# Optimization experiments

Hardware: AMD Instinct MI355X
Metric: run time of the kernel (lower is better)

Reference implementation:

```python
import jax, jax.numpy as jnp
import numpy as np

B, S, H, D_MODEL, D_HEAD = 2, 2048, 12, 768, 64
INIT_RANGE = 0.02
IGNORE = -100000.0


def setup_inputs() -> dict:
    key = jax.random.key(0)
    ks = jax.random.split(key, 11)
    return {
        "normalized_resid_pre_q": jax.random.normal(ks[0], (B, S, H, D_MODEL), jnp.float32),
        "normalized_resid_pre_k": jax.random.normal(ks[1], (B, S, H, D_MODEL), jnp.float32),
        "normalized_resid_pre_v": jax.random.normal(ks[2], (B, S, H, D_MODEL), jnp.float32),
        "W_Q": jax.random.normal(ks[3], (H, D_MODEL, D_HEAD), jnp.float32) * INIT_RANGE,
        "b_Q": jnp.zeros((H, D_HEAD), jnp.float32),
        "W_K": jax.random.normal(ks[4], (H, D_MODEL, D_HEAD), jnp.float32) * INIT_RANGE,
        "b_K": jnp.zeros((H, D_HEAD), jnp.float32),
        "W_V": jax.random.normal(ks[5], (H, D_MODEL, D_HEAD), jnp.float32) * INIT_RANGE,
        "b_V": jnp.zeros((H, D_HEAD), jnp.float32),
        "W_O": jax.random.normal(ks[6], (H, D_HEAD, D_MODEL), jnp.float32) * INIT_RANGE,
        "b_O": jnp.zeros((D_MODEL,), jnp.float32),
    }


def reference(normalized_resid_pre_q, normalized_resid_pre_k, normalized_resid_pre_v,
              W_Q, b_Q, W_K, b_K, W_V, b_V, W_O, b_O):
    n_heads = W_Q.shape[0]
    d_head = W_Q.shape[-1]
    # per-head projections: input already carries a head axis
    q = jnp.einsum("bqhm,hmd->bqhd", normalized_resid_pre_q, W_Q) + b_Q
    k = jnp.einsum("bkhm,hmd->bkhd", normalized_resid_pre_k, W_K) + b_K
    v = jnp.einsum("bkhm,hmd->bkhd", normalized_resid_pre_v, W_V) + b_V
    scores = jnp.einsum("bqhd,bkhd->bhqk", q, k) / jnp.sqrt(jnp.float32(d_head))
    S_q, S_k = scores.shape[-2], scores.shape[-1]
    causal = jnp.triu(jnp.ones((S_q, S_k), bool), k=1)
    scores = jnp.where(causal, jnp.float32(IGNORE), scores)
    pattern = jax.nn.softmax(scores, axis=-1)
    z = jnp.einsum("bhqk,bkhd->bqhd", pattern, v)
    # output keeps the per-head axis; bias split evenly across heads
    attn_out = jnp.einsum("bqhd,hdm->bqhm", z, W_O) + b_O / n_heads
    return attn_out
```

## Files before the change

kernel.cpp:

```cpp
#include <hip/hip_runtime.h>
#include <hip/hip_bf16.h>
#include <stdint.h>

#define H 12
#define S 2048
#define BATCH 2
#define DM 768
#define DH 64

typedef __attribute__((ext_vector_type(4))) float f32x4;
typedef __attribute__((ext_vector_type(8))) short s16x8;

static __device__ __forceinline__ short f2bf(float f) {
  uint32_t u = __builtin_bit_cast(uint32_t, f);
  uint32_t r = (u + 0x7FFFu + ((u >> 16) & 1u)) >> 16;
  return (short)r;
}

static __device__ __forceinline__ s16x8 cvt8(f32x4 a, f32x4 b) {
  s16x8 r;
  r[0] = f2bf(a[0]); r[1] = f2bf(a[1]); r[2] = f2bf(a[2]); r[3] = f2bf(a[3]);
  r[4] = f2bf(b[0]); r[5] = f2bf(b[1]); r[6] = f2bf(b[2]); r[7] = f2bf(b[3]);
  return r;
}

static __device__ __forceinline__ f32x4 zero4() {
  f32x4 v; v[0] = 0.f; v[1] = 0.f; v[2] = 0.f; v[3] = 0.f; return v;
}

static __device__ __forceinline__ int xcd_swz(int lin, int n) {
  int q = n >> 3;
  return (lin & 7) * q + (lin >> 3);
}

#define GLD_LDS16(g, l)                                                              \
  __builtin_amdgcn_global_load_lds((__attribute__((address_space(1))) const void*)(g), \
                                   (__attribute__((address_space(3))) void*)(l), 16, 0, 0)

#define WAITV(N) asm volatile("s_waitcnt vmcnt(" #N ")" ::: "memory")
#define WAITL0() asm volatile("s_waitcnt lgkmcnt(0)" ::: "memory")
#define BAR() __builtin_amdgcn_s_barrier()
#define FENCE() asm volatile("" ::: "memory")

__global__ __launch_bounds__(256) void k_prep(const float* __restrict__ wq,
                                              const float* __restrict__ wk,
                                              const float* __restrict__ wv,
                                              const float* __restrict__ wo,
                                              short* __restrict__ wt,
                                              short* __restrict__ wot) {
  int tid = blockIdx.x * 256 + threadIdx.x;
  int nthr = gridDim.x * 256;
  const int NQKV = 3 * H * DM * DH;
  for (int i = tid; i < NQKV; i += nthr) {
    int n = i & 63;
    int k = (i >> 6) % DM;
    int rest = (i >> 6) / DM;
    int h = rest % H;
    int t = rest / H;
    const float* src = (t == 0 ? wq : t == 1 ? wk : wv);
    float v = src[((size_t)h * DM + k) * DH + n];
    wt[(((size_t)t * H + h) * DH + n) * DM + k] = f2bf(v);
  }
  const int NO = H * DH * DM;
  for (int i = tid; i < NO; i += nthr) {
    int m = i % DM;
    int d = (i / DM) % DH;
    int h = i / (DM * DH);
    wot[((size_t)h * DM + m) * DH + d] = f2bf(wo[((size_t)h * DH + d) * DM + m]);
  }
}

__global__ __launch_bounds__(256) void k_proj(
    const float* __restrict__ xq, const float* __restrict__ xk, const float* __restrict__ xv,
    const float* __restrict__ bq, const float* __restrict__ bk, const float* __restrict__ bv,
    const short* __restrict__ wt,
    short* __restrict__ q_ws, short* __restrict__ k_ws, short* __restrict__ vt_ws) {
  int lin = blockIdx.x + 64 * (blockIdx.y + 12 * blockIdx.z);
  lin = xcd_swz(lin, 64 * 12 * 3);
  const int t = lin / (64 * 12);
  const int h = (lin >> 6) % 12;
  const int b = (lin & 63) >> 5;
  const int q0 = (lin & 31) * 64;

  const float* x = (t == 0 ? xq : t == 1 ? xk : xv);
  const float* xbase = x + ((size_t)(b * S + q0) * H + h) * DM;
  const short* wbase = wt + ((size_t)t * H + h) * (size_t)DH * DM;

  __shared__ float A_sm[2][64 * 64];
  __shared__ short W_sm[2][64 * 64];

  const int tid = threadIdx.x;
  const int w = tid >> 6;
  const int l = tid & 63;
  const int g = l >> 4;
  const int m16 = l & 15;
  const int wswz = ((l & 7) ^ (l >> 3)) * 8;

  const int arow_st = (l >> 4);
  const int apb = (l & 15) * 16;

  f32x4 acc[4];
#pragma unroll
  for (int nt = 0; nt < 4; ++nt) acc[nt] = zero4();

#define PROJ_STAGE(sel, kc)                                                          \
  do {                                                                               \
    _Pragma("unroll") for (int i = 0; i < 4; ++i) {                                  \
      int row = (w * 4 + i) * 4 + arow_st;                                           \
      int colf = (apb ^ ((row & 7) << 4)) >> 2;                                      \
      GLD_LDS16(xbase + (size_t)row * (H * DM) + (kc) * 64 + colf,                   \
                (char*)A_sm + (sel) * 16384 + (w * 4 + i) * 1024);                   \
    }                                                                                \
    _Pragma("unroll") for (int i = 0; i < 2; ++i) {                                  \
      int ch = w * 2 + i;                                                            \
      int n = ch * 8 + (l >> 3);                                                     \
      GLD_LDS16(wbase + (size_t)n * DM + (kc) * 64 + wswz,                           \
                (char*)W_sm + (sel) * 8192 + ch * 1024);                             \
    }                                                                                \
  } while (0)

#define PROJ_COMPUTE(sel)                                                            \
  do {                                                                               \
    const char* Ab = (const char*)A_sm + (sel) * 16384;                              \
    const char* Wb = (const char*)W_sm + (sel) * 8192;                               \
    int arow = 16 * w + m16;                                                         \
    int asw = (arow & 7) << 4;                                                       \
    _Pragma("unroll") for (int c = 0; c < 2; ++c) {                                  \
      f32x4 a0 = *(const f32x4*)(Ab + arow * 256 + ((32 * g + 128 * c) ^ asw));      \
      f32x4 a1 = *(const f32x4*)(Ab + arow * 256 + ((32 * g + 128 * c + 16) ^ asw)); \
      s16x8 afr = cvt8(a0, a1);                                                      \
      int krow = 8 * g + 32 * c;                                                     \
      _Pragma("unroll") for (int nt = 0; nt < 4; ++nt) {                             \
        int n = m16 + 16 * nt;                                                       \
        s16x8 bfr = *(const s16x8*)(Wb + ((n * 128 + krow * 2) ^ ((n & 7) << 4)));   \
        acc[nt] = __builtin_amdgcn_mfma_f32_16x16x32_bf16(afr, bfr, acc[nt], 0, 0, 0); \
      }                                                                              \
    }                                                                                \
  } while (0)

  PROJ_STAGE(0, 0);
#pragma unroll
  for (int kc = 0; kc < 12; ++kc) {
    const int cur = kc & 1;
    if (kc < 11) {
      PROJ_STAGE(cur ^ 1, kc + 1);
      WAITV(6);
    } else {
      WAITV(0);
    }
    BAR(); FENCE();
    PROJ_COMPUTE(cur);
    WAITL0(); BAR(); FENCE();
  }

  const float* bias = (t == 0 ? bq : t == 1 ? bk : bv) + h * DH;
  if (t < 2) {
    short* dst = (t == 0 ? q_ws : k_ws) + (size_t)(b * H + h) * S * DH;
#pragma unroll
    for (int nt = 0; nt < 4; ++nt) {
      int n = 16 * nt + m16;
      float bb = bias[n];
#pragma unroll
      for (int r = 0; r < 4; ++r) {
        int q = q0 + 16 * w + 4 * g + r;
        dst[(size_t)q * DH + n] = f2bf(acc[nt][r] + bb);
      }
    }
  } else {
    short* dst = vt_ws + (size_t)(b * H + h) * DH * S;
#pragma unroll
    for (int nt = 0; nt < 4; ++nt) {
      int n = 16 * nt + m16;
      float bb = bias[n];
#pragma unroll
      for (int r = 0; r < 4; ++r) {
        int q = q0 + 16 * w + 4 * g + r;
        dst[(size_t)n * S + q] = f2bf(acc[nt][r] + bb);
      }
    }
  }
}

__global__ __launch_bounds__(256) void k_attn(const short* __restrict__ q_ws,
                                              const short* __restrict__ k_ws,
                                              const short* __restrict__ vt_ws,
                                              short* __restrict__ z_ws) {
  int lin = blockIdx.x + 32 * (blockIdx.y + 12 * blockIdx.z);
  lin = xcd_swz(lin, 32 * 12 * 2);
  const int q0 = (lin & 31) * 64;
  const int h = (lin >> 5) % 12;
  const int b = lin / (32 * 12);

  const size_t sl = (size_t)(b * H + h) * S * DH;
  const short* qs = q_ws + sl;
  const short* ks = k_ws + sl;
  const short* vs = vt_ws + sl;
  short* zs = z_ws + sl;

  __shared__ short K_sm[2][64 * 64];
  __shared__ short V_sm[2][64 * 64];
  __shared__ short P_sm[4][16 * 72];

  const int tid = threadIdx.x;
  const int w = tid >> 6;
  const int l = tid & 63;
  const int g = l >> 4;
  const int m16 = l & 15;
  const int swz_src = ((l & 7) ^ (l >> 3)) * 8;

#define ATTN_STAGE(sel, kv0)                                                         \
  do {                                                                               \
    _Pragma("unroll") for (int i = 0; i < 2; ++i) {                                  \
      int ch = w * 2 + i;                                                            \
      int row = ch * 8 + (l >> 3);                                                   \
      GLD_LDS16(ks + (size_t)((kv0) + row) * DH + swz_src,                           \
                (char*)K_sm + (sel) * 8192 + ch * 1024);                             \
      GLD_LDS16(vs + (size_t)row * S + (kv0) + swz_src,                              \
                (char*)V_sm + (sel) * 8192 + ch * 1024);                             \
    }                                                                                \
  } while (0)

  s16x8 qf[2];
  {
    int q = q0 + 16 * w + m16;
    qf[0] = *(const s16x8*)(qs + (size_t)q * DH + 8 * g);
    qf[1] = *(const s16x8*)(qs + (size_t)q * DH + 8 * g + 32);
  }

  f32x4 o_acc[4];
  float m_run[4], l_run[4], alpha[4];
#pragma unroll
  for (int nt = 0; nt < 4; ++nt) o_acc[nt] = zero4();
#pragma unroll
  for (int r = 0; r < 4; ++r) { m_run[r] = -3.0e38f; l_run[r] = 0.f; }

  const int ktiles = (q0 >> 6) + 1;
  ATTN_STAGE(0, 0);
  for (int kt = 0; kt < ktiles; ++kt) {
    const int kv0 = kt * 64;
    const int cur = kt & 1;
    if (kt + 1 < ktiles) {
      ATTN_STAGE(cur ^ 1, kv0 + 64);
      WAITV(4);
    } else {
      WAITV(0);
    }
    BAR(); FENCE();

    f32x4 sacc[4];
#pragma unroll
    for (int nt = 0; nt < 4; ++nt) sacc[nt] = zero4();
#pragma unroll
    for (int c = 0; c < 2; ++c) {
      int kr2 = (8 * g + 32 * c) * 2;
#pragma unroll
      for (int nt = 0; nt < 4; ++nt) {
        int row = m16 + 16 * nt;
        s16x8 kf = *(const s16x8*)((const char*)K_sm + cur * 8192 +
                                   ((row * 128 + kr2) ^ ((row & 7) << 4)));
        sacc[nt] = __builtin_amdgcn_mfma_f32_16x16x32_bf16(qf[c], kf, sacc[nt], 0, 0, 0);
      }
    }
    float sv[4][4];
#pragma unroll
    for (int nt = 0; nt < 4; ++nt) {
      int kv = kv0 + 16 * nt + m16;
#pragma unroll
      for (int r = 0; r < 4; ++r) {
        int q = q0 + 16 * w + 4 * g + r;
        float s = sacc[nt][r] * 0.125f;
        sv[nt][r] = (kv > q) ? -1.0e30f : s;
      }
    }
#pragma unroll
    for (int r = 0; r < 4; ++r) {
      float tm = fmaxf(fmaxf(sv[0][r], sv[1][r]), fmaxf(sv[2][r], sv[3][r]));
      tm = fmaxf(tm, __shfl_xor(tm, 1));
      tm = fmaxf(tm, __shfl_xor(tm, 2));
      tm = fmaxf(tm, __shfl_xor(tm, 4));
      tm = fmaxf(tm, __shfl_xor(tm, 8));
      float mn = fmaxf(m_run[r], tm);
      alpha[r] = __expf(m_run[r] - mn);
      m_run[r] = mn;
      float rs = 0.f;
#pragma unroll
      for (int nt = 0; nt < 4; ++nt) {
        float p = __expf(sv[nt][r] - mn);
        sv[nt][r] = p;
        rs += p;
      }
      rs += __shfl_xor(rs, 1);
      rs += __shfl_xor(rs, 2);
      rs += __shfl_xor(rs, 4);
      rs += __shfl_xor(rs, 8);
      l_run[r] = l_run[r] * alpha[r] + rs;
    }
#pragma unroll
    for (int nt = 0; nt < 4; ++nt)
#pragma unroll
      for (int r = 0; r < 4; ++r)
        P_sm[w][(4 * g + r) * 72 + 16 * nt + m16] = f2bf(sv[nt][r]);
#pragma unroll
    for (int nt = 0; nt < 4; ++nt)
#pragma unroll
      for (int r = 0; r < 4; ++r) o_acc[nt][r] *= alpha[r];
#pragma unroll
    for (int c = 0; c < 2; ++c) {
      s16x8 pf = *(const s16x8*)(&P_sm[w][m16 * 72 + 8 * g + 32 * c]);
      int kv2 = (8 * g + 32 * c) * 2;
#pragma unroll
      for (int nt = 0; nt < 4; ++nt) {
        int d = m16 + 16 * nt;
        s16x8 vf = *(const s16x8*)((const char*)V_sm + cur * 8192 +
                                   ((d * 128 + kv2) ^ ((d & 7) << 4)));
        o_acc[nt] = __builtin_amdgcn_mfma_f32_16x16x32_bf16(pf, vf, o_acc[nt], 0, 0, 0);
      }
    }
    WAITL0(); BAR(); FENCE();
  }
#pragma unroll
  for (int nt = 0; nt < 4; ++nt) {
    int d = 16 * nt + m16;
#pragma unroll
    for (int r = 0; r < 4; ++r) {
      int q = q0 + 16 * w + 4 * g + r;
      zs[(size_t)q * DH + d] = f2bf(o_acc[nt][r] / l_run[r]);
    }
  }
}

__global__ __launch_bounds__(256) void k_oproj(const short* __restrict__ z_ws,
                                               const short* __restrict__ wot,
                                               const float* __restrict__ bo,
                                               float* __restrict__ out) {
  int lin = blockIdx.x + 32 * (blockIdx.y + 12 * blockIdx.z);
  lin = xcd_swz(lin, 32 * 12 * 2);
  const int q0 = (lin & 31) * 64;
  const int h = (lin >> 5) % 12;
  const int b = lin / (32 * 12);

  const short* zs = z_ws + (size_t)(b * H + h) * S * DH;
  const short* wos = wot + (size_t)h * DM * DH;

  __shared__ short Z_sm[64 * 64];
  __shared__ short W_sm[2][128 * 64];

  const int tid = threadIdx.x;
  const int w = tid >> 6;
  const int l = tid & 63;
  const int g = l >> 4;
  const int m16 = l & 15;
  const int swz_src = ((l & 7) ^ (l >> 3)) * 8;

#define OPROJ_STAGE_W(sel, n0)                                                       \
  do {                                                                               \
    _Pragma("unroll") for (int i = 0; i < 4; ++i) {                                  \
      int ch = w * 4 + i;                                                            \
      int row = ch * 8 + (l >> 3);                                                   \
      GLD_LDS16(wos + (size_t)((n0) + row) * DH + swz_src,                           \
                (char*)W_sm + (sel) * 16384 + ch * 1024);                            \
    }                                                                                \
  } while (0)

#pragma unroll
  for (int i = 0; i < 2; ++i) {
    int ch = w * 2 + i;
    int row = ch * 8 + (l >> 3);
    GLD_LDS16(zs + (size_t)(q0 + row) * DH + swz_src, (char*)Z_sm + ch * 1024);
  }
  OPROJ_STAGE_W(0, 0);
  WAITV(4);
  BAR(); FENCE();

  s16x8 af[2];
#pragma unroll
  for (int c = 0; c < 2; ++c) {
    int row = 16 * w + m16;
    int kr2 = (8 * g + 32 * c) * 2;
    af[c] = *(const s16x8*)((const char*)Z_sm + ((row * 128 + kr2) ^ ((row & 7) << 4)));
  }

#pragma unroll
  for (int nc = 0; nc < 6; ++nc) {
    const int n0 = nc * 128;
    const int cur = nc & 1;
    if (nc < 5) {
      OPROJ_STAGE_W(cur ^ 1, n0 + 128);
      WAITV(4);
    } else {
      WAITV(0);
    }
    BAR(); FENCE();
    f32x4 acc[8];
#pragma unroll
    for (int nt = 0; nt < 8; ++nt) acc[nt] = zero4();
#pragma unroll
    for (int c = 0; c < 2; ++c) {
      int kr2 = (8 * g + 32 * c) * 2;
#pragma unroll
      for (int nt = 0; nt < 8; ++nt) {
        int row = m16 + 16 * nt;
        s16x8 bf = *(const s16x8*)((const char*)W_sm + cur * 16384 +
                                   ((row * 128 + kr2) ^ ((row & 7) << 4)));
        acc[nt] = __builtin_amdgcn_mfma_f32_16x16x32_bf16(af[c], bf, acc[nt], 0, 0, 0);
      }
    }
#pragma unroll
    for (int nt = 0; nt < 8; ++nt) {
      int m = n0 + 16 * nt + m16;
      float bias = bo[m] * (1.0f / 12.0f);
#pragma unroll
      for (int r = 0; r < 4; ++r) {
        int q = q0 + 16 * w + 4 * g + r;
        out[((size_t)(b * S + q) * H + h) * DM + m] = acc[nt][r] + bias;
      }
    }
    WAITL0(); BAR(); FENCE();
  }
}

extern "C" void kernel_launch(void* const* d_in, const int* in_sizes, int n_in,
                              void* d_out, int out_size, void* d_ws, size_t ws_size,
                              hipStream_t stream) {
  const float* xq = (const float*)d_in[0];
  const float* xk = (const float*)d_in[1];
  const float* xv = (const float*)d_in[2];
  const float* wq = (const float*)d_in[3];
  const float* bq = (const float*)d_in[4];
  const float* wk = (const float*)d_in[5];
  const float* bk = (const float*)d_in[6];
  const float* wv = (const float*)d_in[7];
  const float* bv = (const float*)d_in[8];
  const float* wo = (const float*)d_in[9];
  const float* bo = (const float*)d_in[10];
  float* out = (float*)d_out;

  short* wt = (short*)d_ws;
  short* wot = wt + (size_t)3 * H * DH * DM;
  short* q_ws = wot + (size_t)H * DM * DH;
  short* k_ws = q_ws + (size_t)BATCH * H * S * DH;
  short* vt_ws = k_ws + (size_t)BATCH * H * S * DH;
  short* z_ws = vt_ws + (size_t)BATCH * H * S * DH;

  k_prep<<<dim3(1024), dim3(256), 0, stream>>>(wq, wk, wv, wo, wt, wot);
  k_proj<<<dim3(64, H, 3), dim3(256), 0, stream>>>(xq, xk, xv, bq, bk, bv, wt, q_ws, k_ws, vt_ws);
  k_attn<<<dim3(32, H, BATCH), dim3(256), 0, stream>>>(q_ws, k_ws, vt_ws, z_ws);
  k_oproj<<<dim3(32, H, BATCH), dim3(256), 0, stream>>>(z_ws, wot, bo, out);
}
```

Measured before the change: 264.7 us.

## Stage whole bf16 A row-tile in LDS and halve projection tile size

The projection kernel now loads each block's full 32x768 fp32 activation tile into registers once, converts it to bf16 and stores it in shared memory, instead of double-buffering fp32 A chunks and converting per MFMA step. The block tile shrinks from 64 to 32 rows and the grid doubles, with the four waves split as 2 M-tiles by 2 N-halves. This removes repeated fp32 LDS traffic and conversions from the inner loop and raises block count. In exchange all 24 global loads must finish before any compute, and each block issues W loads for fewer rows, so W is fetched twice as often overall.

Measured after the change: 293.4 us. 10.8% more time.

```diff
diff --git a/kernel.cpp b/kernel.cpp
--- a/kernel.cpp
+++ b/kernel.cpp
@@ -76,17 +76,19 @@
     const short* __restrict__ wt,
     short* __restrict__ q_ws, short* __restrict__ k_ws, short* __restrict__ vt_ws) {
   int lin = blockIdx.x + 64 * (blockIdx.y + 12 * blockIdx.z);
-  lin = xcd_swz(lin, 64 * 12 * 3);
-  const int t = lin / (64 * 12);
-  const int h = (lin >> 6) % 12;
-  const int b = (lin & 63) >> 5;
-  const int q0 = (lin & 31) * 64;
+  int work = xcd_swz(lin, 64 * 12 * 6);
+  const int t = work / 1536;
+  int rem = work - t * 1536;
+  const int b = rem / 768;
+  int r2 = rem - b * 768;
+  const int h = r2 >> 6;
+  const int q0 = (r2 & 63) * 32;
 
   const float* x = (t == 0 ? xq : t == 1 ? xk : xv);
   const float* xbase = x + ((size_t)(b * S + q0) * H + h) * DM;
   const short* wbase = wt + ((size_t)t * H + h) * (size_t)DH * DM;
 
-  __shared__ float A_sm[2][64 * 64];
+  __shared__ short A_sm[32 * 768];
   __shared__ short W_sm[2][64 * 64];
 
   const int tid = threadIdx.x;
@@ -96,21 +98,8 @@
   const int m16 = l & 15;
   const int wswz = ((l & 7) ^ (l >> 3)) * 8;
 
-  const int arow_st = (l >> 4);
-  const int apb = (l & 15) * 16;
-
-  f32x4 acc[4];
-#pragma unroll
-  for (int nt = 0; nt < 4; ++nt) acc[nt] = zero4();
-
-#define PROJ_STAGE(sel, kc)                                                          \
+#define PROJ_STAGE_W(sel, kc)                                                        \
   do {                                                                               \
-    _Pragma("unroll") for (int i = 0; i < 4; ++i) {                                  \
-      int row = (w * 4 + i) * 4 + arow_st;                                           \
-      int colf = (apb ^ ((row & 7) << 4)) >> 2;                                      \
-      GLD_LDS16(xbase + (size_t)row * (H * DM) + (kc) * 64 + colf,                   \
-                (char*)A_sm + (sel) * 16384 + (w * 4 + i) * 1024);                   \
-    }                                                                                \
     _Pragma("unroll") for (int i = 0; i < 2; ++i) {                                  \
       int ch = w * 2 + i;                                                            \
       int n = ch * 8 + (l >> 3);                                                     \
@@ -119,37 +108,61 @@
     }                                                                                \
   } while (0)
 
-#define PROJ_COMPUTE(sel)                                                            \
-  do {                                                                               \
-    const char* Ab = (const char*)A_sm + (sel) * 16384;                              \
-    const char* Wb = (const char*)W_sm + (sel) * 8192;                               \
-    int arow = 16 * w + m16;                                                         \
-    int asw = (arow & 7) << 4;                                                       \
-    _Pragma("unroll") for (int c = 0; c < 2; ++c) {                                  \
-      f32x4 a0 = *(const f32x4*)(Ab + arow * 256 + ((32 * g + 128 * c) ^ asw));      \
-      f32x4 a1 = *(const f32x4*)(Ab + arow * 256 + ((32 * g + 128 * c + 16) ^ asw)); \
-      s16x8 afr = cvt8(a0, a1);                                                      \
-      int krow = 8 * g + 32 * c;                                                     \
-      _Pragma("unroll") for (int nt = 0; nt < 4; ++nt) {                             \
-        int n = m16 + 16 * nt;                                                       \
-        s16x8 bfr = *(const s16x8*)(Wb + ((n * 128 + krow * 2) ^ ((n & 7) << 4)));   \
-        acc[nt] = __builtin_amdgcn_mfma_f32_16x16x32_bf16(afr, bfr, acc[nt], 0, 0, 0); \
-      }                                                                              \
-    }                                                                                \
-  } while (0)
-
-  PROJ_STAGE(0, 0);
+  {
+    const int row_l = tid >> 3;
+    const int s8 = tid & 7;
+    const float* arow = xbase + (size_t)row_l * (H * DM) + s8 * 8;
+
+    PROJ_STAGE_W(0, 0);
+
+    f32x4 Ar[24];
+#pragma unroll
+    for (int j = 0; j < 12; ++j) {
+      Ar[2 * j] = *(const f32x4*)(arow + j * 64);
+      Ar[2 * j + 1] = *(const f32x4*)(arow + j * 64 + 4);
+    }
+    const int abase = row_l * 1536;
+    const int aswz = (row_l & 7) << 4;
+#pragma unroll
+    for (int j = 0; j < 12; ++j) {
+      s16x8 v = cvt8(Ar[2 * j], Ar[2 * j + 1]);
+      *(s16x8*)((char*)A_sm + abase + ((s8 * 16 + j * 128) ^ aswz)) = v;
+    }
+    WAITL0(); BAR(); FENCE();
+  }
+
+  const int mt = w >> 1;
+  const int np = w & 1;
+  const int rowA = 16 * mt + m16;
+  const int abase2 = rowA * 1536;
+  const int aswz2 = (m16 & 7) << 4;
+
+  f32x4 acc[2];
+  acc[0] = zero4(); acc[1] = zero4();
+
 #pragma unroll
   for (int kc = 0; kc < 12; ++kc) {
     const int cur = kc & 1;
     if (kc < 11) {
-      PROJ_STAGE(cur ^ 1, kc + 1);
-      WAITV(6);
+      PROJ_STAGE_W(cur ^ 1, kc + 1);
+      WAITV(2);
     } else {
       WAITV(0);
     }
     BAR(); FENCE();
-    PROJ_COMPUTE(cur);
+    const char* Wb = (const char*)W_sm + cur * 8192;
+#pragma unroll
+    for (int c = 0; c < 2; ++c) {
+      s16x8 afr = *(const s16x8*)((const char*)A_sm + abase2 +
+                                  ((16 * g + 64 * c + 128 * kc) ^ aswz2));
+      int kr2 = (8 * g + 32 * c) * 2;
+#pragma unroll
+      for (int j2 = 0; j2 < 2; ++j2) {
+        int n = 16 * (2 * np + j2) + m16;
+        s16x8 bfr = *(const s16x8*)(Wb + ((n * 128 + kr2) ^ ((n & 7) << 4)));
+        acc[j2] = __builtin_amdgcn_mfma_f32_16x16x32_bf16(afr, bfr, acc[j2], 0, 0, 0);
+      }
+    }
     WAITL0(); BAR(); FENCE();
   }
 
@@ -157,25 +170,25 @@
   if (t < 2) {
     short* dst = (t == 0 ? q_ws : k_ws) + (size_t)(b * H + h) * S * DH;
 #pragma unroll
-    for (int nt = 0; nt < 4; ++nt) {
-      int n = 16 * nt + m16;
+    for (int j2 = 0; j2 < 2; ++j2) {
+      int n = 16 * (2 * np + j2) + m16;
       float bb = bias[n];
 #pragma unroll
       for (int r = 0; r < 4; ++r) {
-        int q = q0 + 16 * w + 4 * g + r;
-        dst[(size_t)q * DH + n] = f2bf(acc[nt][r] + bb);
+        int q = q0 + 16 * mt + 4 * g + r;
+        dst[(size_t)q * DH + n] = f2bf(acc[j2][r] + bb);
       }
     }
   } else {
     short* dst = vt_ws + (size_t)(b * H + h) * DH * S;
 #pragma unroll
-    for (int nt = 0; nt < 4; ++nt) {
-      int n = 16 * nt + m16;
+    for (int j2 = 0; j2 < 2; ++j2) {
+      int n = 16 * (2 * np + j2) + m16;
       float bb = bias[n];
 #pragma unroll
       for (int r = 0; r < 4; ++r) {
-        int q = q0 + 16 * w + 4 * g + r;
-        dst[(size_t)n * S + q] = f2bf(acc[nt][r] + bb);
+        int q = q0 + 16 * mt + 4 * g + r;
+        dst[(size_t)n * S + q] = f2bf(acc[j2][r] + bb);
       }
     }
   }
@@ -443,7 +456,7 @@
   short* z_ws = vt_ws + (size_t)BATCH * H * S * DH;
 
   k_prep<<<dim3(1024), dim3(256), 0, stream>>>(wq, wk, wv, wo, wt, wot);
-  k_proj<<<dim3(64, H, 3), dim3(256), 0, stream>>>(xq, xk, xv, bq, bk, bv, wt, q_ws, k_ws, vt_ws);
+  k_proj<<<dim3(64, H, 6), dim3(256), 0, stream>>>(xq, xk, xv, bq, bk, bv, wt, q_ws, k_ws, vt_ws);
   k_attn<<<dim3(32, H, BATCH), dim3(256), 0, stream>>>(q_ws, k_ws, vt_ws, z_ws);
   k_oproj<<<dim3(32, H, BATCH), dim3(256), 0, stream>>>(z_ws, wot, bo, out);
 }
```

## Restructure QKV projection to stream contiguous row slabs across all heads per block

Applied to the files above, without the earlier changes.

The projection kernel now assigns each block 16 token rows of one input tensor and loops over all 12 heads, instead of a 64x64 tile for a single head. For each head it stages the full 768-wide fp32 row slab into LDS, double-buffered, and streams weight tiles through a separate double buffer. Biases are preloaded into LDS, and V-transpose stores are packed into 4-wide vectors. The aim is contiguous, fully coalesced reads of the large fp32 activations. In exchange, each block re-reads far more weight data, issues only two MFMAs per barrier, and uses about 107KB of LDS, which limits occupancy to one block per CU.

After: 419.4 us. 58.4% more time.

```diff
diff --git a/kernel.cpp b/kernel.cpp
--- a/kernel.cpp
+++ b/kernel.cpp
@@ -9,6 +9,7 @@
 #define DH 64
 
 typedef __attribute__((ext_vector_type(4))) float f32x4;
+typedef __attribute__((ext_vector_type(4))) short s16x4;
 typedef __attribute__((ext_vector_type(8))) short s16x8;
 
 static __device__ __forceinline__ short f2bf(float f) {
@@ -75,19 +76,18 @@
     const float* __restrict__ bq, const float* __restrict__ bk, const float* __restrict__ bv,
     const short* __restrict__ wt,
     short* __restrict__ q_ws, short* __restrict__ k_ws, short* __restrict__ vt_ws) {
-  int lin = blockIdx.x + 64 * (blockIdx.y + 12 * blockIdx.z);
-  lin = xcd_swz(lin, 64 * 12 * 3);
-  const int t = lin / (64 * 12);
-  const int h = (lin >> 6) % 12;
-  const int b = (lin & 63) >> 5;
-  const int q0 = (lin & 31) * 64;
+  int work = xcd_swz(blockIdx.x, 768);
+  const int t = work >> 8;
+  const int b = (work >> 7) & 1;
+  const int qc = work & 127;
 
   const float* x = (t == 0 ? xq : t == 1 ? xk : xv);
-  const float* xbase = x + ((size_t)(b * S + q0) * H + h) * DM;
-  const short* wbase = wt + ((size_t)t * H + h) * (size_t)DH * DM;
-
-  __shared__ float A_sm[2][64 * 64];
+  const float* xslab = x + (size_t)(b * S + qc * 16) * (H * DM);
+  const short* wtt = wt + (size_t)t * H * DH * DM;
+
+  __shared__ float A_sm[2][16 * 768];
   __shared__ short W_sm[2][64 * 64];
+  __shared__ float bias_lds[H * DH];
 
   const int tid = threadIdx.x;
   const int w = tid >> 6;
@@ -95,90 +95,90 @@
   const int g = l >> 4;
   const int m16 = l & 15;
   const int wswz = ((l & 7) ^ (l >> 3)) * 8;
-
-  const int arow_st = (l >> 4);
-  const int apb = (l & 15) * 16;
-
-  f32x4 acc[4];
-#pragma unroll
-  for (int nt = 0; nt < 4; ++nt) acc[nt] = zero4();
-
-#define PROJ_STAGE(sel, kc)                                                          \
+  const int n2 = w * 16 + m16;
+
+  {
+    const float* bp = (t == 0 ? bq : t == 1 ? bk : bv);
+    for (int i = tid; i < H * DH; i += 256) bias_lds[i] = bp[i];
+  }
+
+#define STAGE_A(sel, hh)                                                             \
   do {                                                                               \
-    _Pragma("unroll") for (int i = 0; i < 4; ++i) {                                  \
-      int row = (w * 4 + i) * 4 + arow_st;                                           \
-      int colf = (apb ^ ((row & 7) << 4)) >> 2;                                      \
-      GLD_LDS16(xbase + (size_t)row * (H * DM) + (kc) * 64 + colf,                   \
-                (char*)A_sm + (sel) * 16384 + (w * 4 + i) * 1024);                   \
+    _Pragma("unroll") for (int j = 0; j < 12; ++j) {                                 \
+      int row = w * 4 + j / 3;                                                       \
+      int seg = j % 3;                                                               \
+      int srccol = ((seg * 1024 + l * 16) ^ ((row & 7) << 4)) >> 2;                  \
+      GLD_LDS16(xslab + (size_t)row * (H * DM) + (size_t)(hh) * DM + srccol,         \
+                (char*)A_sm + (sel) * 49152 + row * 3072 + seg * 1024);              \
     }                                                                                \
+  } while (0)
+
+#define STAGE_W(sel, hh, kc)                                                         \
+  do {                                                                               \
     _Pragma("unroll") for (int i = 0; i < 2; ++i) {                                  \
       int ch = w * 2 + i;                                                            \
       int n = ch * 8 + (l >> 3);                                                     \
-      GLD_LDS16(wbase + (size_t)n * DM + (kc) * 64 + wswz,                           \
+      GLD_LDS16(wtt + (size_t)(hh) * (DH * DM) + (size_t)n * DM + (kc) * 64 + wswz,  \
                 (char*)W_sm + (sel) * 8192 + ch * 1024);                             \
     }                                                                                \
   } while (0)
 
-#define PROJ_COMPUTE(sel)                                                            \
-  do {                                                                               \
-    const char* Ab = (const char*)A_sm + (sel) * 16384;                              \
-    const char* Wb = (const char*)W_sm + (sel) * 8192;                               \
-    int arow = 16 * w + m16;                                                         \
-    int asw = (arow & 7) << 4;                                                       \
-    _Pragma("unroll") for (int c = 0; c < 2; ++c) {                                  \
-      f32x4 a0 = *(const f32x4*)(Ab + arow * 256 + ((32 * g + 128 * c) ^ asw));      \
-      f32x4 a1 = *(const f32x4*)(Ab + arow * 256 + ((32 * g + 128 * c + 16) ^ asw)); \
-      s16x8 afr = cvt8(a0, a1);                                                      \
-      int krow = 8 * g + 32 * c;                                                     \
-      _Pragma("unroll") for (int nt = 0; nt < 4; ++nt) {                             \
-        int n = m16 + 16 * nt;                                                       \
-        s16x8 bfr = *(const s16x8*)(Wb + ((n * 128 + krow * 2) ^ ((n & 7) << 4)));   \
-        acc[nt] = __builtin_amdgcn_mfma_f32_16x16x32_bf16(afr, bfr, acc[nt], 0, 0, 0); \
-      }                                                                              \
-    }                                                                                \
-  } while (0)
-
-  PROJ_STAGE(0, 0);
-#pragma unroll
-  for (int kc = 0; kc < 12; ++kc) {
-    const int cur = kc & 1;
-    if (kc < 11) {
-      PROJ_STAGE(cur ^ 1, kc + 1);
-      WAITV(6);
-    } else {
-      WAITV(0);
-    }
-    BAR(); FENCE();
-    PROJ_COMPUTE(cur);
-    WAITL0(); BAR(); FENCE();
-  }
-
-  const float* bias = (t == 0 ? bq : t == 1 ? bk : bv) + h * DH;
-  if (t < 2) {
-    short* dst = (t == 0 ? q_ws : k_ws) + (size_t)(b * H + h) * S * DH;
-#pragma unroll
-    for (int nt = 0; nt < 4; ++nt) {
-      int n = 16 * nt + m16;
-      float bb = bias[n];
-#pragma unroll
-      for (int r = 0; r < 4; ++r) {
-        int q = q0 + 16 * w + 4 * g + r;
-        dst[(size_t)q * DH + n] = f2bf(acc[nt][r] + bb);
-      }
-    }
-  } else {
-    short* dst = vt_ws + (size_t)(b * H + h) * DH * S;
-#pragma unroll
-    for (int nt = 0; nt < 4; ++nt) {
-      int n = 16 * nt + m16;
-      float bb = bias[n];
-#pragma unroll
-      for (int r = 0; r < 4; ++r) {
-        int q = q0 + 16 * w + 4 * g + r;
-        dst[(size_t)n * S + q] = f2bf(acc[nt][r] + bb);
-      }
-    }
-  }
+  STAGE_W(0, 0, 0);
+  STAGE_A(0, 0);
+  WAITL0(); BAR(); FENCE();
+
+  short* dstqk_base = (t == 0 ? q_ws : k_ws) + (size_t)b * H * S * DH;
+  f32x4 acc = zero4();
+
+  for (int h = 0; h < 12; ++h) {
+#pragma unroll
+    for (int kc = 0; kc < 12; ++kc) {
+      const int G = h * 12 + kc;
+      if (kc == 0) {
+        int hh = h + 1; if (hh > 11) hh = 11;
+        STAGE_A((h + 1) & 1, hh);
+      }
+      {
+        int Gn = G + 1; if (Gn > 143) Gn = 143;
+        STAGE_W((G + 1) & 1, Gn / 12, Gn % 12);
+      }
+      WAITV(14);
+      BAR(); FENCE();
+      if (kc == 0) acc = zero4();
+      const char* Ab = (const char*)A_sm + (h & 1) * 49152;
+      const char* Wb = (const char*)W_sm + (G & 1) * 8192;
+      const int aswz = (m16 & 7) << 4;
+#pragma unroll
+      for (int qk = 0; qk < 2; ++qk) {
+        int fb = (kc * 2 + qk) * 128 + g * 32;
+        f32x4 a0 = *(const f32x4*)(Ab + m16 * 3072 + (fb ^ aswz));
+        f32x4 a1 = *(const f32x4*)(Ab + m16 * 3072 + ((fb + 16) ^ aswz));
+        s16x8 afr = cvt8(a0, a1);
+        s16x8 bfr = *(const s16x8*)(Wb + ((n2 * 128 + 16 * g + 64 * qk) ^ ((m16 & 7) << 4)));
+        acc = __builtin_amdgcn_mfma_f32_16x16x32_bf16(afr, bfr, acc, 0, 0, 0);
+      }
+      if (kc == 11) {
+        float bb = bias_lds[h * DH + n2];
+        if (t < 2) {
+          short* dst = dstqk_base + (size_t)h * S * DH;
+#pragma unroll
+          for (int r = 0; r < 4; ++r) {
+            int q = qc * 16 + 4 * g + r;
+            dst[(size_t)q * DH + n2] = f2bf(acc[r] + bb);
+          }
+        } else {
+          short* dst = vt_ws + (size_t)(b * H + h) * DH * S;
+          s16x4 pk;
+          pk.x = f2bf(acc[0] + bb); pk.y = f2bf(acc[1] + bb);
+          pk.z = f2bf(acc[2] + bb); pk.w = f2bf(acc[3] + bb);
+          *(s16x4*)(dst + (size_t)n2 * S + qc * 16 + 4 * g) = pk;
+        }
+      }
+      WAITL0(); BAR(); FENCE();
+    }
+  }
+#undef STAGE_A
+#undef STAGE_W
 }
 
 __global__ __launch_bounds__(256) void k_attn(const short* __restrict__ q_ws,
@@ -443,7 +443,7 @@
   short* z_ws = vt_ws + (size_t)BATCH * H * S * DH;
 
   k_prep<<<dim3(1024), dim3(256), 0, stream>>>(wq, wk, wv, wo, wt, wot);
-  k_proj<<<dim3(64, H, 3), dim3(256), 0, stream>>>(xq, xk, xv, bq, bk, bv, wt, q_ws, k_ws, vt_ws);
+  k_proj<<<dim3(768), dim3(256), 0, stream>>>(xq, xk, xv, bq, bk, bv, wt, q_ws, k_ws, vt_ws);
   k_attn<<<dim3(32, H, BATCH), dim3(256), 0, stream>>>(q_ws, k_ws, vt_ws, z_ws);
   k_oproj<<<dim3(32, H, BATCH), dim3(256), 0, stream>>>(z_ws, wot, bo, out);
 }
```

## Fuse output projection into attention kernel and reorder block scheduling

Applied to the files above, without the earlier changes.

Merges the attention and output-projection kernels so the normalized attention output is written straight to shared memory and projected in place, which removes the z workspace round trip and one launch. The block index mapping is changed so that blocks sharing a head land on the same XCD, and attention tiles are issued longest-first (reversed q tile) to reduce causal tail imbalance. The W_O staging is cut to 64-column chunks to fit in the reused K/V shared buffers, and the bias is cached in LDS. Risks include tighter vmcnt wait counts and a longer-running fused kernel holding more registers.

After: 219.0 us. 17.3% less time.

```diff
diff --git a/kernel.cpp b/kernel.cpp
--- a/kernel.cpp
+++ b/kernel.cpp
@@ -9,6 +9,7 @@
 #define DH 64
 
 typedef __attribute__((ext_vector_type(4))) float f32x4;
+typedef __attribute__((ext_vector_type(4))) short s16x4;
 typedef __attribute__((ext_vector_type(8))) short s16x8;
 
 static __device__ __forceinline__ short f2bf(float f) {
@@ -26,11 +27,6 @@
 
 static __device__ __forceinline__ f32x4 zero4() {
   f32x4 v; v[0] = 0.f; v[1] = 0.f; v[2] = 0.f; v[3] = 0.f; return v;
-}
-
-static __device__ __forceinline__ int xcd_swz(int lin, int n) {
-  int q = n >> 3;
-  return (lin & 7) * q + (lin >> 3);
 }
 
 #define GLD_LDS16(g, l)                                                              \
@@ -75,12 +71,15 @@
     const float* __restrict__ bq, const float* __restrict__ bk, const float* __restrict__ bv,
     const short* __restrict__ wt,
     short* __restrict__ q_ws, short* __restrict__ k_ws, short* __restrict__ vt_ws) {
-  int lin = blockIdx.x + 64 * (blockIdx.y + 12 * blockIdx.z);
-  lin = xcd_swz(lin, 64 * 12 * 3);
-  const int t = lin / (64 * 12);
-  const int h = (lin >> 6) % 12;
-  const int b = (lin & 63) >> 5;
-  const int q0 = (lin & 31) * 64;
+  const int u = blockIdx.x;
+  const int xcd = u & 7;
+  const int slot = u >> 3;
+  const int r = (slot / 12) * 8 + xcd;
+  const int h = slot % 12;
+  const int t = r / 64;
+  const int rb = r % 64;
+  const int b = rb >> 5;
+  const int q0 = (rb & 31) * 64;
 
   const float* x = (t == 0 ? xq : t == 1 ? xk : xv);
   const float* xbase = x + ((size_t)(b * S + q0) * H + h) * DM;
@@ -161,9 +160,9 @@
       int n = 16 * nt + m16;
       float bb = bias[n];
 #pragma unroll
-      for (int r = 0; r < 4; ++r) {
-        int q = q0 + 16 * w + 4 * g + r;
-        dst[(size_t)q * DH + n] = f2bf(acc[nt][r] + bb);
+      for (int r2 = 0; r2 < 4; ++r2) {
+        int q = q0 + 16 * w + 4 * g + r2;
+        dst[(size_t)q * DH + n] = f2bf(acc[nt][r2] + bb);
       }
     }
   } else {
@@ -173,29 +172,33 @@
       int n = 16 * nt + m16;
       float bb = bias[n];
 #pragma unroll
-      for (int r = 0; r < 4; ++r) {
-        int q = q0 + 16 * w + 4 * g + r;
-        dst[(size_t)n * S + q] = f2bf(acc[nt][r] + bb);
-      }
-    }
-  }
-}
-
-__global__ __launch_bounds__(256) void k_attn(const short* __restrict__ q_ws,
-                                              const short* __restrict__ k_ws,
-                                              const short* __restrict__ vt_ws,
-                                              short* __restrict__ z_ws) {
-  int lin = blockIdx.x + 32 * (blockIdx.y + 12 * blockIdx.z);
-  lin = xcd_swz(lin, 32 * 12 * 2);
-  const int q0 = (lin & 31) * 64;
-  const int h = (lin >> 5) % 12;
-  const int b = lin / (32 * 12);
+      for (int r2 = 0; r2 < 4; ++r2) {
+        int q = q0 + 16 * w + 4 * g + r2;
+        dst[(size_t)n * S + q] = f2bf(acc[nt][r2] + bb);
+      }
+    }
+  }
+}
+
+__global__ __launch_bounds__(256) void k_attn_o(const short* __restrict__ q_ws,
+                                                const short* __restrict__ k_ws,
+                                                const short* __restrict__ vt_ws,
+                                                const short* __restrict__ wot,
+                                                const float* __restrict__ bo,
+                                                float* __restrict__ out) {
+  const int u = blockIdx.x;
+  const int xcd = u & 7;
+  const int slot = u >> 3;
+  const int r = (slot / 12) * 8 + xcd;
+  const int h = slot % 12;
+  const int b = r >> 5;
+  const int qtile = 31 - (r & 31);
+  const int q0 = qtile * 64;
 
   const size_t sl = (size_t)(b * H + h) * S * DH;
   const short* qs = q_ws + sl;
   const short* ks = k_ws + sl;
   const short* vs = vt_ws + sl;
-  short* zs = z_ws + sl;
 
   __shared__ short K_sm[2][64 * 64];
   __shared__ short V_sm[2][64 * 64];
@@ -232,9 +235,9 @@
 #pragma unroll
   for (int nt = 0; nt < 4; ++nt) o_acc[nt] = zero4();
 #pragma unroll
-  for (int r = 0; r < 4; ++r) { m_run[r] = -3.0e38f; l_run[r] = 0.f; }
-
-  const int ktiles = (q0 >> 6) + 1;
+  for (int rr = 0; rr < 4; ++rr) { m_run[rr] = -3.0e38f; l_run[rr] = 0.f; }
+
+  const int ktiles = qtile + 1;
   ATTN_STAGE(0, 0);
   for (int kt = 0; kt < ktiles; ++kt) {
     const int kv0 = kt * 64;
@@ -266,44 +269,44 @@
     for (int nt = 0; nt < 4; ++nt) {
       int kv = kv0 + 16 * nt + m16;
 #pragma unroll
-      for (int r = 0; r < 4; ++r) {
-        int q = q0 + 16 * w + 4 * g + r;
-        float s = sacc[nt][r] * 0.125f;
-        sv[nt][r] = (kv > q) ? -1.0e30f : s;
-      }
-    }
-#pragma unroll
-    for (int r = 0; r < 4; ++r) {
-      float tm = fmaxf(fmaxf(sv[0][r], sv[1][r]), fmaxf(sv[2][r], sv[3][r]));
+      for (int rr = 0; rr < 4; ++rr) {
+        int q = q0 + 16 * w + 4 * g + rr;
+        float s = sacc[nt][rr] * 0.125f;
+        sv[nt][rr] = (kv > q) ? -1.0e30f : s;
+      }
+    }
+#pragma unroll
+    for (int rr = 0; rr < 4; ++rr) {
+      float tm = fmaxf(fmaxf(sv[0][rr], sv[1][rr]), fmaxf(sv[2][rr], sv[3][rr]));
       tm = fmaxf(tm, __shfl_xor(tm, 1));
       tm = fmaxf(tm, __shfl_xor(tm, 2));
       tm = fmaxf(tm, __shfl_xor(tm, 4));
       tm = fmaxf(tm, __shfl_xor(tm, 8));
-      float mn = fmaxf(m_run[r], tm);
-      alpha[r] = __expf(m_run[r] - mn);
-      m_run[r] = mn;
+      float mn = fmaxf(m_run[rr], tm);
+      alpha[rr] = __expf(m_run[rr] - mn);
+      m_run[rr] = mn;
       float rs = 0.f;
 #pragma unroll
       for (int nt = 0; nt < 4; ++nt) {
-        float p = __expf(sv[nt][r] - mn);
-        sv[nt][r] = p;
+        float p = __expf(sv[nt][rr] - mn);
+        sv[nt][rr] = p;
         rs += p;
       }
       rs += __shfl_xor(rs, 1);
       rs += __shfl_xor(rs, 2);
       rs += __shfl_xor(rs, 4);
       rs += __shfl_xor(rs, 8);
-      l_run[r] = l_run[r] * alpha[r] + rs;
+      l_run[rr] = l_run[rr] * alpha[rr] + rs;
     }
 #pragma unroll
     for (int nt = 0; nt < 4; ++nt)
 #pragma unroll
-      for (int r = 0; r < 4; ++r)
-        P_sm[w][(4 * g + r) * 72 + 16 * nt + m16] = f2bf(sv[nt][r]);
+      for (int rr = 0; rr < 4; ++rr)
+        P_sm[w][(4 * g + rr) * 72 + 16 * nt + m16] = f2bf(sv[nt][rr]);
 #pragma unroll
     for (int nt = 0; nt < 4; ++nt)
 #pragma unroll
-      for (int r = 0; r < 4; ++r) o_acc[nt][r] *= alpha[r];
+      for (int rr = 0; rr < 4; ++rr) o_acc[nt][rr] *= alpha[rr];
 #pragma unroll
     for (int c = 0; c < 2; ++c) {
       s16x8 pf = *(const s16x8*)(&P_sm[w][m16 * 72 + 8 * g + 32 * c]);
@@ -318,59 +321,35 @@
     }
     WAITL0(); BAR(); FENCE();
   }
-#pragma unroll
-  for (int nt = 0; nt < 4; ++nt) {
-    int d = 16 * nt + m16;
-#pragma unroll
-    for (int r = 0; r < 4; ++r) {
-      int q = q0 + 16 * w + 4 * g + r;
-      zs[(size_t)q * DH + d] = f2bf(o_acc[nt][r] / l_run[r]);
-    }
-  }
-}
-
-__global__ __launch_bounds__(256) void k_oproj(const short* __restrict__ z_ws,
-                                               const short* __restrict__ wot,
-                                               const float* __restrict__ bo,
-                                               float* __restrict__ out) {
-  int lin = blockIdx.x + 32 * (blockIdx.y + 12 * blockIdx.z);
-  lin = xcd_swz(lin, 32 * 12 * 2);
-  const int q0 = (lin & 31) * 64;
-  const int h = (lin >> 5) % 12;
-  const int b = lin / (32 * 12);
-
-  const short* zs = z_ws + (size_t)(b * H + h) * S * DH;
+
+  short* Z_sm = (short*)K_sm;
+  char* WO_sm = (char*)V_sm;
+  float* bo_lds = (float*)P_sm;
   const short* wos = wot + (size_t)h * DM * DH;
 
-  __shared__ short Z_sm[64 * 64];
-  __shared__ short W_sm[2][128 * 64];
-
-  const int tid = threadIdx.x;
-  const int w = tid >> 6;
-  const int l = tid & 63;
-  const int g = l >> 4;
-  const int m16 = l & 15;
-  const int swz_src = ((l & 7) ^ (l >> 3)) * 8;
-
-#define OPROJ_STAGE_W(sel, n0)                                                       \
+#define STAGE_WO(sel, nc)                                                            \
   do {                                                                               \
-    _Pragma("unroll") for (int i = 0; i < 4; ++i) {                                  \
-      int ch = w * 4 + i;                                                            \
+    _Pragma("unroll") for (int i = 0; i < 2; ++i) {                                  \
+      int ch = w * 2 + i;                                                            \
       int row = ch * 8 + (l >> 3);                                                   \
-      GLD_LDS16(wos + (size_t)((n0) + row) * DH + swz_src,                           \
-                (char*)W_sm + (sel) * 16384 + ch * 1024);                            \
+      GLD_LDS16(wos + (size_t)((nc) * 64 + row) * DH + swz_src,                      \
+                WO_sm + (sel) * 8192 + ch * 1024);                                   \
     }                                                                                \
   } while (0)
 
-#pragma unroll
-  for (int i = 0; i < 2; ++i) {
-    int ch = w * 2 + i;
-    int row = ch * 8 + (l >> 3);
-    GLD_LDS16(zs + (size_t)(q0 + row) * DH + swz_src, (char*)Z_sm + ch * 1024);
-  }
-  OPROJ_STAGE_W(0, 0);
-  WAITV(4);
-  BAR(); FENCE();
+  STAGE_WO(0, 0);
+  for (int i = tid; i < DM; i += 256) bo_lds[i] = bo[i] * (1.0f / 12.0f);
+#pragma unroll
+  for (int nt = 0; nt < 4; ++nt) {
+#pragma unroll
+    for (int rr = 0; rr < 4; ++rr) {
+      int row = 16 * w + 4 * g + rr;
+      int d = 16 * nt + m16;
+      int byte = (row * 128 + d * 2) ^ ((row & 7) << 4);
+      *(short*)((char*)Z_sm + byte) = f2bf(o_acc[nt][rr] / l_run[rr]);
+    }
+  }
+  WAITL0(); BAR(); FENCE();
 
   s16x8 af[2];
 #pragma unroll
@@ -381,42 +360,44 @@
   }
 
 #pragma unroll
-  for (int nc = 0; nc < 6; ++nc) {
-    const int n0 = nc * 128;
+  for (int nc = 0; nc < 12; ++nc) {
     const int cur = nc & 1;
-    if (nc < 5) {
-      OPROJ_STAGE_W(cur ^ 1, n0 + 128);
-      WAITV(4);
+    if (nc < 11) {
+      STAGE_WO(cur ^ 1, nc + 1);
+      if (nc == 0) { WAITV(2); }
+      else        { WAITV(18); }
     } else {
       WAITV(0);
     }
     BAR(); FENCE();
-    f32x4 acc[8];
-#pragma unroll
-    for (int nt = 0; nt < 8; ++nt) acc[nt] = zero4();
+    f32x4 acc[4];
+#pragma unroll
+    for (int nt = 0; nt < 4; ++nt) acc[nt] = zero4();
 #pragma unroll
     for (int c = 0; c < 2; ++c) {
       int kr2 = (8 * g + 32 * c) * 2;
 #pragma unroll
-      for (int nt = 0; nt < 8; ++nt) {
+      for (int nt = 0; nt < 4; ++nt) {
         int row = m16 + 16 * nt;
-        s16x8 bf = *(const s16x8*)((const char*)W_sm + cur * 16384 +
+        s16x8 bf = *(const s16x8*)(WO_sm + cur * 8192 +
                                    ((row * 128 + kr2) ^ ((row & 7) << 4)));
         acc[nt] = __builtin_amdgcn_mfma_f32_16x16x32_bf16(af[c], bf, acc[nt], 0, 0, 0);
       }
     }
 #pragma unroll
-    for (int nt = 0; nt < 8; ++nt) {
-      int m = n0 + 16 * nt + m16;
-      float bias = bo[m] * (1.0f / 12.0f);
-#pragma unroll
-      for (int r = 0; r < 4; ++r) {
-        int q = q0 + 16 * w + 4 * g + r;
-        out[((size_t)(b * S + q) * H + h) * DM + m] = acc[nt][r] + bias;
+    for (int nt = 0; nt < 4; ++nt) {
+      int m = nc * 64 + 16 * nt + m16;
+      float bias = bo_lds[m];
+#pragma unroll
+      for (int rr = 0; rr < 4; ++rr) {
+        int q = q0 + 16 * w + 4 * g + rr;
+        out[((size_t)(b * S + q) * H + h) * DM + m] = acc[nt][rr] + bias;
       }
     }
     WAITL0(); BAR(); FENCE();
   }
+#undef STAGE_WO
+#undef ATTN_STAGE
 }
 
 extern "C" void kernel_launch(void* const* d_in, const int* in_sizes, int n_in,
@@ -440,10 +421,8 @@
   short* q_ws = wot + (size_t)H * DM * DH;
   short* k_ws = q_ws + (size_t)BATCH * H * S * DH;
   short* vt_ws = k_ws + (size_t)BATCH * H * S * DH;
-  short* z_ws = vt_ws + (size_t)BATCH * H * S * DH;
 
   k_prep<<<dim3(1024), dim3(256), 0, stream>>>(wq, wk, wv, wo, wt, wot);
-  k_proj<<<dim3(64, H, 3), dim3(256), 0, stream>>>(xq, xk, xv, bq, bk, bv, wt, q_ws, k_ws, vt_ws);
-  k_attn<<<dim3(32, H, BATCH), dim3(256), 0, stream>>>(q_ws, k_ws, vt_ws, z_ws);
-  k_oproj<<<dim3(32, H, BATCH), dim3(256), 0, stream>>>(z_ws, wot, bo, out);
-}
+  k_proj<<<dim3(2304), dim3(256), 0, stream>>>(xq, xk, xv, bq, bk, bv, wt, q_ws, k_ws, vt_ws);
+  k_attn_o<<<dim3(768), dim3(256), 0, stream>>>(q_ws, k_ws, vt_ws, wot, bo, out);
+}
```
